# Performance work log

Measured on AMD Instinct MI355X. Metric: run time of the kernel, lower is better.

## Reference

```python
import jax, jax.numpy as jnp
import numpy as np

L, M, K = 13, 12, 5
ODD_KS = tuple(range(1, K + 1, 2))  # (1, 3, 5) -> n_odd_order = 3
NK = len(ODD_KS)


def setup_inputs() -> dict:
    key = jax.random.key(0)
    k1, k2, k3, k4 = jax.random.split(key, 4)
    B, T = 16, 8192
    x = jax.random.normal(k1, (B, T, 2), dtype=jnp.float32)
    h_0 = jnp.zeros((B, 16), dtype=jnp.float32)  # unused by forward (API compat)
    A_kl = jax.random.normal(k2, (L, NK), dtype=jnp.float32) * 0.1
    B_klm = jax.random.normal(k3, (L, M, NK), dtype=jnp.float32) * 0.1
    C_klm = jax.random.normal(k4, (L, M, NK), dtype=jnp.float32) * 0.1
    return {"x": x, "h_0": h_0, "A_kl": A_kl, "B_klm": B_klm, "C_klm": C_klm}


def _gmp_forward(x, A_kl, B_klm, C_klm):
    # x: [B, T, 2] real/imag -> complex signal
    Bsz, T, _ = x.shape
    xc = jax.lax.complex(x[..., 0], x[..., 1])  # [B, T]

    # Circular window indices (equivalent to torch cat+unfold in the original).
    t = jnp.arange(T)[:, None, None]
    l = jnp.arange(L)[None, :, None]
    m = jnp.arange(M + 1)[None, None, :]
    # 2nd term pads with the LAST (L+M-1) samples at the front -> index shift back
    idx2 = (t + l + m - (L + M - 1)) % T  # [T, L, M+1]
    # 3rd term pads with the FIRST (L+M-1) samples at the end -> forward wrap
    idx3 = (t + l + m) % T                # [T, L, M+1]

    x2 = xc[:, idx2]  # [B, T, L, M+1] complex
    x3 = xc[:, idx3]  # [B, T, L, M+1] complex
    # First-term window x[t-(L-1)+l] equals the m=M element of the 2nd-term window.
    x1 = x2[..., -1]  # [B, T, L]

    # --- term 1: sum_{l,k} A[l,k] * x1 * |x1|^k ---
    a1 = jnp.abs(x1)                                        # [B,T,L]
    p1 = jnp.stack([a1 ** k for k in ODD_KS], axis=-1)       # [B,T,L,NK] real
    c1 = jnp.einsum('btlk,lk->btl', p1, A_kl)                # real coefficient
    term1 = jnp.sum(x1 * c1, axis=-1)                        # [B,T] complex

    # --- term 2: sum_{l,m,k} B[l,m,k] * x2[...,M] * |x2[...,m]|^k ---
    a2 = jnp.abs(x2[..., :-1])                               # [B,T,L,M]
    p2 = jnp.stack([a2 ** k for k in ODD_KS], axis=-1)       # [B,T,L,M,NK]
    c2 = jnp.einsum('btlmk,lmk->btl', p2, B_klm)             # sum over m,k too
    term2 = jnp.sum(x1 * c2, axis=-1)                        # multiplier is x2[...,-1]==x1

    # --- term 3: same structure with forward-lag windows and C ---
    x3_last = x3[..., -1]                                    # [B,T,L]
    a3 = jnp.abs(x3[..., :-1])                               # [B,T,L,M]
    p3 = jnp.stack([a3 ** k for k in ODD_KS], axis=-1)       # [B,T,L,M,NK]
    c3 = jnp.einsum('btlmk,lmk->btl', p3, C_klm)
    term3 = jnp.sum(x3_last * c3, axis=-1)

    s = term1 + term2 + term3                                # [B,T] complex
    return jnp.stack([jnp.real(s), jnp.imag(s)], axis=-1)    # [B,T,2] float32


def reference(x, h_0, A_kl, B_klm, C_klm):
    # h_0 is accepted but unused, matching the torch module.
    return _gmp_forward(x, A_kl, B_klm, C_klm)
```

## Files before the change

### kernel.cpp

```cpp
#include <hip/hip_runtime.h>
#include <math.h>

#define LL    13
#define MM    12
#define NKK   3
#define BLOCK 256
#define HALO  24
#define WIN   (BLOCK + 2*HALO)
#define DMAX  25
#define NW    (DMAX * LL)


__global__ __launch_bounds__(BLOCK)
void gmp_kernel(const float* __restrict__ x,
                const float* __restrict__ Ac,
                const float* __restrict__ Bc,
                const float* __restrict__ Cc,
                float* __restrict__ out,
                int T, int tilesPerB)
{
    __shared__ float4 sP[WIN];
    __shared__ float2 sZ[WIN];
    __shared__ float4 sWB[NW];
    __shared__ float4 sWC[NW];

    const int tid = threadIdx.x;
    const int b   = blockIdx.x / tilesPerB;
    const int t0  = (blockIdx.x % tilesPerB) * BLOCK;

    const float* xb = x + (size_t)b * T * 2;

    for (int j = tid; j < WIN; j += BLOCK) {
        int t = t0 - HALO + j;
        if (t < 0)  t += T;
        if (t >= T) t -= T;
        const float2 z = *(const float2*)(xb + 2 * t);
        float a2 = z.x * z.x + z.y * z.y;
        float a  = sqrtf(a2);
        sZ[j] = z;
        sP[j] = make_float4(a, a * a2, a * a2 * a2, 0.0f);
    }

    for (int idx = tid; idx < NW; idx += BLOCK) {
        const int d = idx / LL;
        const int l = idx - d * LL;
        const int m = d - l;
        float4 wb = make_float4(0.f, 0.f, 0.f, 0.f);
        float4 wc = make_float4(0.f, 0.f, 0.f, 0.f);
        if (m >= 0 && m <= MM) {
            const float* s = (m == MM) ? (Ac + l * NKK)
                                       : (Bc + (l * MM + m) * NKK);
            wb = make_float4(s[0], s[1], s[2], 0.f);
        }
        if (m >= 0 && m < MM) {
            const float* s = Cc + (l * MM + m) * NKK;
            wc = make_float4(s[0], s[1], s[2], 0.f);
        }
        sWB[idx] = wb;
        sWC[idx] = wc;
    }
    __syncthreads();

    float cB[LL], cC[LL];
    #pragma unroll
    for (int l = 0; l < LL; ++l) { cB[l] = 0.f; cC[l] = 0.f; }

    #pragma unroll
    for (int d = 0; d < DMAX; ++d) {
        const float4 p = sP[tid + d];
        const float4 q = sP[tid + d + 24];
        #pragma unroll
        for (int l = 0; l < LL; ++l) {
            const int m = d - l;
            if (m >= 0 && m <= MM) {
                const float4 w = sWB[d * LL + l];
                cB[l] += w.x * p.x + w.y * p.y + w.z * p.z;
            }
            if (m >= 0 && m < MM) {
                const float4 w = sWC[d * LL + l];
                cC[l] += w.x * q.x + w.y * q.y + w.z * q.z;
            }
        }
    }

    float sr = 0.0f, si = 0.0f;
    #pragma unroll
    for (int l = 0; l < LL; ++l) {
        const float2 z1 = sZ[tid + l + 12];
        const float2 z3 = sZ[tid + l + 36];
        sr += z1.x * cB[l] + z3.x * cC[l];
        si += z1.y * cB[l] + z3.y * cC[l];
    }

    const int t = t0 + tid;
    if (t < T) {
        float2* op = (float2*)(out + ((size_t)b * T + t) * 2);
        *op = make_float2(sr, si);
    }
}

extern "C" void kernel_launch(void* const* d_in, const int* in_sizes, int n_in,
                              void* d_out, int out_size, void* d_ws, size_t ws_size,
                              hipStream_t stream)
{
    const float* x  = (const float*)d_in[0];
    const float* Ac = (const float*)d_in[2];
    const float* Bc = (const float*)d_in[3];
    const float* Cc = (const float*)d_in[4];
    float* out = (float*)d_out;

    const int Bsz = in_sizes[1] / 16;
    const int T   = in_sizes[0] / (2 * Bsz);
    const int tilesPerB = (T + BLOCK - 1) / BLOCK;

    dim3 grid(Bsz * tilesPerB);
    dim3 block(BLOCK);
    gmp_kernel<<<grid, block, 0, stream>>>(x, Ac, Bc, Cc, out, T, tilesPerB);
}
```

Measured before the change: 73.68 us.

## Split per-output convolution across four wavefronts with shared-memory reduction

Each block now produces 64 outputs instead of 256. Its four wavefronts each take one half of the B or C window convolution for the same outputs, and the partial complex sums are combined through shared memory. The intent is to cut per-thread register pressure and serial work per thread, which should raise occupancy and widen the grid. In exchange it adds a second barrier, recomputes the halo for four times as many blocks, and reloads the weight tables into shared memory in every block.

```diff
diff --git a/kernel.cpp b/kernel.cpp
--- a/kernel.cpp
+++ b/kernel.cpp
@@ -4,12 +4,36 @@
 #define LL    13
 #define MM    12
 #define NKK   3
+#define OUTS  64
 #define BLOCK 256
 #define HALO  24
-#define WIN   (BLOCK + 2*HALO)
-#define DMAX  25
-#define NW    (DMAX * LL)
+#define WIN   (OUTS + 2*HALO)
+#define NWB   (25 * LL)
+#define NWC   (24 * LL)
 
+__shared__ float4 sP[WIN];
+__shared__ float2 sZ[WIN];
+__shared__ float4 sWB[NWB];
+__shared__ float4 sWC[NWC];
+__shared__ float2 sAcc[4][OUTS];
+
+template<int D0, int D1, int POFS>
+__device__ __forceinline__ void conv_half(const float4* __restrict__ sW,
+                                          int o, float c[LL])
+{
+    #pragma unroll
+    for (int d = D0; d < D1; ++d) {
+        const float4 p = sP[o + POFS + d];
+        #pragma unroll
+        for (int l = 0; l < LL; ++l) {
+            const int m = d - l;
+            if (m >= 0 && m <= MM) {
+                const float4 w = sW[d * LL + l];
+                c[l] += w.x * p.x + w.y * p.y + w.z * p.z;
+            }
+        }
+    }
+}
 
 __global__ __launch_bounds__(BLOCK)
 void gmp_kernel(const float* __restrict__ x,
@@ -19,83 +43,82 @@
                 float* __restrict__ out,
                 int T, int tilesPerB)
 {
-    __shared__ float4 sP[WIN];
-    __shared__ float2 sZ[WIN];
-    __shared__ float4 sWB[NW];
-    __shared__ float4 sWC[NW];
-
     const int tid = threadIdx.x;
     const int b   = blockIdx.x / tilesPerB;
-    const int t0  = (blockIdx.x % tilesPerB) * BLOCK;
+    const int t0  = (blockIdx.x % tilesPerB) * OUTS;
 
     const float* xb = x + (size_t)b * T * 2;
 
-    for (int j = tid; j < WIN; j += BLOCK) {
-        int t = t0 - HALO + j;
+    if (tid < WIN) {
+        int t = t0 - HALO + tid;
         if (t < 0)  t += T;
         if (t >= T) t -= T;
         const float2 z = *(const float2*)(xb + 2 * t);
         float a2 = z.x * z.x + z.y * z.y;
         float a  = sqrtf(a2);
-        sZ[j] = z;
-        sP[j] = make_float4(a, a * a2, a * a2 * a2, 0.0f);
+        sZ[tid] = z;
+        sP[tid] = make_float4(a, a * a2, a * a2 * a2, 0.0f);
     }
 
-    for (int idx = tid; idx < NW; idx += BLOCK) {
+    for (int idx = tid; idx < NWB; idx += BLOCK) {
         const int d = idx / LL;
         const int l = idx - d * LL;
         const int m = d - l;
-        float4 wb = make_float4(0.f, 0.f, 0.f, 0.f);
-        float4 wc = make_float4(0.f, 0.f, 0.f, 0.f);
+        float4 w = make_float4(0.f, 0.f, 0.f, 0.f);
         if (m >= 0 && m <= MM) {
             const float* s = (m == MM) ? (Ac + l * NKK)
                                        : (Bc + (l * MM + m) * NKK);
-            wb = make_float4(s[0], s[1], s[2], 0.f);
+            w = make_float4(s[0], s[1], s[2], 0.f);
         }
+        sWB[idx] = w;
+    }
+    for (int idx = tid; idx < NWC; idx += BLOCK) {
+        const int d = idx / LL;
+        const int l = idx - d * LL;
+        const int m = d - l;
+        float4 w = make_float4(0.f, 0.f, 0.f, 0.f);
         if (m >= 0 && m < MM) {
             const float* s = Cc + (l * MM + m) * NKK;
-            wc = make_float4(s[0], s[1], s[2], 0.f);
+            w = make_float4(s[0], s[1], s[2], 0.f);
         }
-        sWB[idx] = wb;
-        sWC[idx] = wc;
+        sWC[idx] = w;
     }
     __syncthreads();
 
-    float cB[LL], cC[LL];
+    const int o    = tid & 63;
+    const int role = tid >> 6;
+
+    float c[LL];
     #pragma unroll
-    for (int l = 0; l < LL; ++l) { cB[l] = 0.f; cC[l] = 0.f; }
+    for (int l = 0; l < LL; ++l) c[l] = 0.f;
 
-    #pragma unroll
-    for (int d = 0; d < DMAX; ++d) {
-        const float4 p = sP[tid + d];
-        const float4 q = sP[tid + d + 24];
-        #pragma unroll
-        for (int l = 0; l < LL; ++l) {
-            const int m = d - l;
-            if (m >= 0 && m <= MM) {
-                const float4 w = sWB[d * LL + l];
-                cB[l] += w.x * p.x + w.y * p.y + w.z * p.z;
-            }
-            if (m >= 0 && m < MM) {
-                const float4 w = sWC[d * LL + l];
-                cC[l] += w.x * q.x + w.y * q.y + w.z * q.z;
-            }
-        }
-    }
+    if      (role == 0) conv_half< 0, 13,  0>(sWB, o, c);
+    else if (role == 1) conv_half<13, 25,  0>(sWB, o, c);
+    else if (role == 2) conv_half< 0, 12, 24>(sWC, o, c);
+    else                conv_half<12, 24, 24>(sWC, o, c);
 
-    float sr = 0.0f, si = 0.0f;
+    const int zofs = (role < 2) ? 12 : 36;
+    float sr = 0.f, si = 0.f;
     #pragma unroll
     for (int l = 0; l < LL; ++l) {
-        const float2 z1 = sZ[tid + l + 12];
-        const float2 z3 = sZ[tid + l + 36];
-        sr += z1.x * cB[l] + z3.x * cC[l];
-        si += z1.y * cB[l] + z3.y * cC[l];
+        const float2 z = sZ[o + l + zofs];
+        sr += z.x * c[l];
+        si += z.y * c[l];
     }
+    sAcc[role][o] = make_float2(sr, si);
+    __syncthreads();
 
-    const int t = t0 + tid;
-    if (t < T) {
-        float2* op = (float2*)(out + ((size_t)b * T + t) * 2);
-        *op = make_float2(sr, si);
+    if (tid < OUTS) {
+        const float2 a0 = sAcc[0][tid];
+        const float2 a1 = sAcc[1][tid];
+        const float2 a2 = sAcc[2][tid];
+        const float2 a3 = sAcc[3][tid];
+        const int t = t0 + tid;
+        if (t < T) {
+            float2* op = (float2*)(out + ((size_t)b * T + t) * 2);
+            *op = make_float2(a0.x + a1.x + a2.x + a3.x,
+                              a0.y + a1.y + a2.y + a3.y);
+        }
     }
 }
 
@@ -111,7 +134,7 @@
 
     const int Bsz = in_sizes[1] / 16;
     const int T   = in_sizes[0] / (2 * Bsz);
-    const int tilesPerB = (T + BLOCK - 1) / BLOCK;
+    const int tilesPerB = (T + OUTS - 1) / OUTS;
 
     dim3 grid(Bsz * tilesPerB);
     dim3 block(BLOCK);
```

Result: slower. 78.12 us (+6.0%).
